# Optimization experiments

Hardware: AMD Instinct MI355X
Metric: run time of the kernel (lower is better)

The kernel has to match this reference:

```python
import math
import jax, jax.numpy as jnp
import numpy as np

H = 8
C_HIDDEN = 32
C_Q = 256


def setup_inputs() -> dict:
    key = jax.random.key(0)
    ks = jax.random.split(key, 9)
    B, S, Q, K = 1, 128, 256, 256
    q_x = jax.random.normal(ks[0], (B, S, Q, C_Q), dtype=jnp.float32)
    kv_x = jax.random.normal(ks[1], (B, S, K, C_Q), dtype=jnp.float32)
    bias1 = jax.random.normal(ks[2], (B, S, 1, 1, K), dtype=jnp.float32)
    bias2 = jax.random.normal(ks[3], (B, 1, H, Q, K), dtype=jnp.float32)
    scale = 1.0 / math.sqrt(C_Q)
    wq = jax.random.normal(ks[4], (H * C_HIDDEN, C_Q), dtype=jnp.float32) * scale
    wk = jax.random.normal(ks[5], (H * C_HIDDEN, C_Q), dtype=jnp.float32) * scale
    wv = jax.random.normal(ks[6], (H * C_HIDDEN, C_Q), dtype=jnp.float32) * scale
    wg = jax.random.normal(ks[7], (H * C_HIDDEN, C_Q), dtype=jnp.float32) * scale
    wo = jax.random.normal(ks[8], (C_Q, H * C_HIDDEN), dtype=jnp.float32) * scale
    return {"q_x": q_x, "kv_x": kv_x, "bias1": bias1, "bias2": bias2,
            "wq": wq, "wk": wk, "wv": wv, "wg": wg, "wo": wo}


def _split_heads(x):
    # [..., L, H*c] -> [..., H, L, c]
    y = x.reshape(x.shape[:-1] + (H, C_HIDDEN))
    return jnp.moveaxis(y, -2, -3)


def reference(q_x, kv_x, bias1, bias2, wq, wk, wv, wg, wo):
    # QKV projections (no bias), per-head split, scale q by 1/sqrt(c_hidden)
    q = _split_heads(q_x @ wq.T) / math.sqrt(C_HIDDEN)   # [B,S,H,Q,c]
    k = _split_heads(kv_x @ wk.T)                         # [B,S,H,K,c]
    v = _split_heads(kv_x @ wv.T)                         # [B,S,H,K,c]
    # attention logits with additive biases folded in
    a = jnp.einsum('...hqc,...hkc->...hqk', q, k) + bias1 + bias2
    a = jax.nn.softmax(a, axis=-1)
    o = jnp.einsum('...hqk,...hkc->...hqc', a, v)         # [B,S,H,Q,c]
    o = jnp.moveaxis(o, -3, -2)                           # [B,S,Q,H,c]
    # sigmoid gating from query data
    g = jax.nn.sigmoid(q_x @ wg.T)                        # [B,S,Q,H*c]
    g = g.reshape(g.shape[:-1] + (H, C_HIDDEN))
    o = o * g
    o = o.reshape(o.shape[:-2] + (H * C_HIDDEN,))         # flatten heads
    return o @ wo.T                                       # [B,S,Q,C_Q]
```

## Files before the change

### kernel.cpp

```cpp
#include <hip/hip_runtime.h>
#include <math.h>

#define S_DIM 128
#define H_DIM 8
#define M_TOT (S_DIM * 256)

typedef unsigned short ushort_t;
typedef unsigned int   uint32;
typedef __bf16  v8bf  __attribute__((ext_vector_type(8)));
typedef float   v4f   __attribute__((ext_vector_type(4)));

__device__ inline ushort_t f2b(float x) {
    unsigned int u = __float_as_uint(x);
    u += 0x7fffu + ((u >> 16) & 1u);
    return (ushort_t)(u >> 16);
}
__device__ inline float b2f(ushort_t h) {
    return __uint_as_float(((unsigned int)h) << 16);
}

#define GLDS16(gp, lp) __builtin_amdgcn_global_load_lds( \
    (const __attribute__((address_space(1))) void*)(gp), \
    (__attribute__((address_space(3))) void*)(lp), 16, 0, 0)

__global__ __launch_bounds__(256) void split_x(
    const float* __restrict__ xq, const float* __restrict__ xkv,
    ushort_t* __restrict__ hi, ushort_t* __restrict__ lo)
{
    const size_t BUF4 = (size_t)M_TOT * 64;
    const float* src = blockIdx.y ? xkv : xq;
    size_t base = (size_t)blockIdx.y * BUF4;
    int i = blockIdx.x * 256 + threadIdx.x;
    float4 v = ((const float4*)src)[i];
    ushort4 h, l;
    h.x = f2b(v.x); l.x = f2b(v.x - b2f(h.x));
    h.y = f2b(v.y); l.y = f2b(v.y - b2f(h.y));
    h.z = f2b(v.z); l.z = f2b(v.z - b2f(h.z));
    h.w = f2b(v.w); l.w = f2b(v.w - b2f(h.w));
    ((ushort4*)hi)[base + i] = h;
    ((ushort4*)lo)[base + i] = l;
}

__global__ __launch_bounds__(256) void split_w(
    const float* __restrict__ w0, const float* __restrict__ w1,
    const float* __restrict__ w2, const float* __restrict__ w3,
    const float* __restrict__ w4,
    ushort_t* __restrict__ hi, ushort_t* __restrict__ lo)
{
    const float* src;
    switch (blockIdx.y) {
        case 0: src = w0; break; case 1: src = w1; break;
        case 2: src = w2; break; case 3: src = w3; break;
        default: src = w4; break;
    }
    int i = blockIdx.x * 256 + threadIdx.x;
    float4 v = ((const float4*)src)[i];
    ushort4 h, l;
    h.x = f2b(v.x); l.x = f2b(v.x - b2f(h.x));
    h.y = f2b(v.y); l.y = f2b(v.y - b2f(h.y));
    h.z = f2b(v.z); l.z = f2b(v.z - b2f(h.z));
    h.w = f2b(v.w); l.w = f2b(v.w - b2f(h.w));
    size_t base = (size_t)blockIdx.y * 16384;
    ((ushort4*)hi)[base + i] = h;
    ((ushort4*)lo)[base + i] = l;
}


__global__ __launch_bounds__(256) void gemm_proj(
    const ushort_t* __restrict__ Xhi, const ushort_t* __restrict__ Xlo,
    const ushort_t* __restrict__ Whi4, const ushort_t* __restrict__ Wlo4,
    ushort_t* __restrict__ qh, ushort_t* __restrict__ ql,
    ushort_t* __restrict__ kh, ushort_t* __restrict__ kl,
    float* __restrict__ g_out,
    ushort_t* __restrict__ vh,
    float qscale)
{
    __shared__ ushort_t lds[4][128 * 32];

    const int z    = blockIdx.z;
    const int L    = blockIdx.x + 4 * blockIdx.y;
    const int mti  = ((L >> 5) << 3) + (L & 7);
    const int nti  = (L >> 3) & 3;
    const int t    = threadIdx.x;
    const int l    = t & 63;
    const int wv   = t >> 6;
    const int wm   = wv & 1;
    const int wn   = wv >> 1;
    const int idx  = l & 15;
    const int quad = l >> 4;
    const int m0   = mti * 128;
    const int n0   = nti * 128;

    const size_t BUF = (size_t)M_TOT * 256;
    const ushort_t* Ahi = Xhi + (size_t)z * BUF;
    const ushort_t* Alo = Xlo + (size_t)z * BUF;
    const ushort_t* Whi = Whi4 + (size_t)z * 131072;
    const ushort_t* Wlo = Wlo4 + (size_t)z * 131072;
    const float scale = z ? 1.f : qscale;

    const ushort_t* srcs[4] = { Ahi + (size_t)m0 * 256, Alo + (size_t)m0 * 256,
                                Whi + (size_t)n0 * 256, Wlo + (size_t)n0 * 256 };

    v4f acc[4][4];
    #pragma unroll
    for (int i = 0; i < 4; ++i)
        #pragma unroll
        for (int j = 0; j < 4; ++j) acc[i][j] = (v4f){0.f, 0.f, 0.f, 0.f};

    for (int k0 = 0; k0 < 256; k0 += 32) {
        #pragma unroll
        for (int b = 0; b < 4; ++b) {
            #pragma unroll
            for (int i = 0; i < 2; ++i) {
                const int sb   = wv * 128 + i * 64;
                const int slot = sb + l;
                const int row  = slot >> 2;
                const int gseg = ((slot & 3) - (row >> 1)) & 3;
                const ushort_t* g = srcs[b] + (size_t)row * 256 + k0 + gseg * 8;
                GLDS16(g, &lds[b][sb * 8]);
            }
        }
        __builtin_amdgcn_s_waitcnt(0);
        __syncthreads();

        v8bf ah[4], al[4], bh[4], bl[4];
        #pragma unroll
        for (int mt = 0; mt < 4; ++mt) {
            const int r   = wm * 64 + mt * 16 + idx;
            const int off = r * 32 + (((quad + (r >> 1)) & 3) << 3);
            ah[mt] = *(const v8bf*)&lds[0][off];
            al[mt] = *(const v8bf*)&lds[1][off];
        }
        #pragma unroll
        for (int nt = 0; nt < 4; ++nt) {
            const int r   = wn * 64 + nt * 16 + idx;
            const int off = r * 32 + (((quad + (r >> 1)) & 3) << 3);
            bh[nt] = *(const v8bf*)&lds[2][off];
            bl[nt] = *(const v8bf*)&lds[3][off];
        }

        #pragma unroll
        for (int mt = 0; mt < 4; ++mt)
            #pragma unroll
            for (int nt = 0; nt < 4; ++nt) {
                acc[mt][nt] = __builtin_amdgcn_mfma_f32_16x16x32_bf16(ah[mt], bh[nt], acc[mt][nt], 0, 0, 0);
                acc[mt][nt] = __builtin_amdgcn_mfma_f32_16x16x32_bf16(al[mt], bh[nt], acc[mt][nt], 0, 0, 0);
                acc[mt][nt] = __builtin_amdgcn_mfma_f32_16x16x32_bf16(ah[mt], bl[nt], acc[mt][nt], 0, 0, 0);
            }
        __syncthreads();
    }

    ushort_t* dsth = z ? kh : qh;
    ushort_t* dstl = z ? kl : ql;

    #pragma unroll
    for (int mt = 0; mt < 4; ++mt) {
        const int mbase = m0 + wm * 64 + mt * 16 + quad * 4;
        const int s = mbase >> 8, r8 = mbase & 255;
        #pragma unroll
        for (int nt = 0; nt < 4; ++nt) {
            const int gcol = n0 + wn * 64 + nt * 16 + idx;
            if (gcol < 256) {
                const int hh = gcol >> 5, c = gcol & 31;
                const size_t di = (((size_t)(s * 8 + hh) * 256) + r8) * 32 + c;
                #pragma unroll
                for (int r = 0; r < 4; ++r) {
                    const float val = acc[mt][nt][r] * scale;
                    const ushort_t hv = f2b(val);
                    dsth[di + (size_t)r * 32] = hv;
                    dstl[di + (size_t)r * 32] = f2b(val - b2f(hv));
                }
            } else if (z == 0) {
                const int gc = gcol - 256;
                #pragma unroll
                for (int r = 0; r < 4; ++r)
                    g_out[(size_t)(mbase + r) * 256 + gc] = acc[mt][nt][r];
            } else {
                const int gc = gcol - 256, hh = gc >> 5, c = gc & 31;
                ushort4 hv4;
                #pragma unroll
                for (int r = 0; r < 4; ++r)
                    ((ushort_t*)&hv4)[r] = f2b(acc[mt][nt][r]);
                const size_t di = (((size_t)(s * 8 + hh) * 32) + c) * 256 + r8;
                *(ushort4*)&vh[di] = hv4;
            }
        }
    }
}

__global__ __launch_bounds__(256) void gemm_out(
    const ushort_t* __restrict__ Ah, const ushort_t* __restrict__ Whi,
    const ushort_t* __restrict__ Wlo, float* __restrict__ Cf)
{
    __shared__ ushort_t lds[3][128 * 32];

    const int L    = blockIdx.x + 2 * blockIdx.y;
    const int mti  = ((L >> 4) << 3) + (L & 7);
    const int nti  = (L >> 3) & 1;
    const int t    = threadIdx.x;
    const int l    = t & 63;
    const int wv   = t >> 6;
    const int wm   = wv & 1;
    const int wn   = wv >> 1;
    const int idx  = l & 15;
    const int quad = l >> 4;
    const int m0   = mti * 128;
    const int n0   = nti * 128;

    const ushort_t* srcs[3] = { Ah + (size_t)m0 * 256,
                                Whi + (size_t)n0 * 256, Wlo + (size_t)n0 * 256 };

    v4f acc[4][4];
    #pragma unroll
    for (int i = 0; i < 4; ++i)
        #pragma unroll
        for (int j = 0; j < 4; ++j) acc[i][j] = (v4f){0.f, 0.f, 0.f, 0.f};

    for (int k0 = 0; k0 < 256; k0 += 32) {
        #pragma unroll
        for (int b = 0; b < 3; ++b) {
            #pragma unroll
            for (int i = 0; i < 2; ++i) {
                const int sb   = wv * 128 + i * 64;
                const int slot = sb + l;
                const int row  = slot >> 2;
                const int gseg = ((slot & 3) - (row >> 1)) & 3;
                const ushort_t* g = srcs[b] + (size_t)row * 256 + k0 + gseg * 8;
                GLDS16(g, &lds[b][sb * 8]);
            }
        }
        __builtin_amdgcn_s_waitcnt(0);
        __syncthreads();

        v8bf ah[4], bh[4], bl[4];
        #pragma unroll
        for (int mt = 0; mt < 4; ++mt) {
            const int r   = wm * 64 + mt * 16 + idx;
            const int off = r * 32 + (((quad + (r >> 1)) & 3) << 3);
            ah[mt] = *(const v8bf*)&lds[0][off];
        }
        #pragma unroll
        for (int nt = 0; nt < 4; ++nt) {
            const int r   = wn * 64 + nt * 16 + idx;
            const int off = r * 32 + (((quad + (r >> 1)) & 3) << 3);
            bh[nt] = *(const v8bf*)&lds[1][off];
            bl[nt] = *(const v8bf*)&lds[2][off];
        }

        #pragma unroll
        for (int mt = 0; mt < 4; ++mt)
            #pragma unroll
            for (int nt = 0; nt < 4; ++nt) {
                acc[mt][nt] = __builtin_amdgcn_mfma_f32_16x16x32_bf16(ah[mt], bh[nt], acc[mt][nt], 0, 0, 0);
                acc[mt][nt] = __builtin_amdgcn_mfma_f32_16x16x32_bf16(ah[mt], bl[nt], acc[mt][nt], 0, 0, 0);
            }
        __syncthreads();
    }

    #pragma unroll
    for (int mt = 0; mt < 4; ++mt) {
        #pragma unroll
        for (int nt = 0; nt < 4; ++nt) {
            const int gcol = n0 + wn * 64 + nt * 16 + idx;
            #pragma unroll
            for (int r = 0; r < 4; ++r) {
                const int grow = m0 + wm * 64 + mt * 16 + quad * 4 + r;
                Cf[(size_t)grow * 256 + gcol] = acc[mt][nt][r];
            }
        }
    }
}

__global__ __launch_bounds__(256, 2) void attn_mfma(
    const ushort_t* __restrict__ qh, const ushort_t* __restrict__ ql,
    const ushort_t* __restrict__ kh, const ushort_t* __restrict__ kl,
    const ushort_t* __restrict__ vth,
    const float* __restrict__ b1, const float* __restrict__ b2,
    const float* __restrict__ gbuf,
    ushort_t* __restrict__ oh)
{
    __shared__ __align__(16) uint32 pbuf[4][64 * 36];
    __shared__ __align__(16) float  lbuf[4][64 * 4];
    __shared__ __align__(16) float  invl[4][64];

    const int sh = blockIdx.x, s = sh >> 3, h = sh & 7;
    const int t = threadIdx.x, l = t & 63, w = t >> 6;
    const int idx = l & 15, quad = l >> 4;

    const size_t shb = (size_t)sh * 8192;
    const ushort_t* qhp = qh + shb;
    const ushort_t* qlp = ql + shb;
    const ushort_t* khp = kh + shb;
    const ushort_t* klp = kl + shb;
    const ushort_t* vhp = vth + shb;
    const float* b1p = b1 + (size_t)s * 256;
    const float* b2p = b2 + (size_t)h * 65536;

    v8bf qfh[4], qfl[4];
    #pragma unroll
    for (int nt = 0; nt < 4; ++nt) {
        const int off = (w * 64 + nt * 16 + idx) * 32 + quad * 8;
        qfh[nt] = *(const v8bf*)(qhp + off);
        qfl[nt] = *(const v8bf*)(qlp + off);
    }

    v4f oacc[4][2];
    #pragma unroll
    for (int mt = 0; mt < 4; ++mt) {
        oacc[mt][0] = (v4f){0.f, 0.f, 0.f, 0.f};
        oacc[mt][1] = (v4f){0.f, 0.f, 0.f, 0.f};
    }
    float lrun[4] = {0.f, 0.f, 0.f, 0.f};

    for (int c4 = 0; c4 < 4; ++c4) {
        const int ak0 = c4 * 64;

        v8bf kfh[4], kfl[4];
        #pragma unroll
        for (int at = 0; at < 4; ++at) {
            const int off = (ak0 + at * 16 + idx) * 32 + quad * 8;
            kfh[at] = *(const v8bf*)(khp + off);
            kfl[at] = *(const v8bf*)(klp + off);
        }

        v4f sacc[4][4];
        #pragma unroll
        for (int at = 0; at < 4; ++at)
            #pragma unroll
            for (int nt = 0; nt < 4; ++nt)
                sacc[at][nt] = (v4f){0.f, 0.f, 0.f, 0.f};
        #pragma unroll
        for (int at = 0; at < 4; ++at)
            #pragma unroll
            for (int nt = 0; nt < 4; ++nt) {
                sacc[at][nt] = __builtin_amdgcn_mfma_f32_16x16x32_bf16(kfh[at], qfh[nt], sacc[at][nt], 0, 0, 0);
                sacc[at][nt] = __builtin_amdgcn_mfma_f32_16x16x32_bf16(kfl[at], qfh[nt], sacc[at][nt], 0, 0, 0);
                sacc[at][nt] = __builtin_amdgcn_mfma_f32_16x16x32_bf16(kfh[at], qfl[nt], sacc[at][nt], 0, 0, 0);
            }

        v4f b1v[4];
        #pragma unroll
        for (int at = 0; at < 4; ++at)
            b1v[at] = *(const v4f*)(b1p + ak0 + at * 16 + quad * 4);

        #pragma unroll
        for (int at = 0; at < 4; ++at)
            #pragma unroll
            for (int nt = 0; nt < 4; ++nt) {
                const int q = w * 64 + nt * 16 + idx;
                v4f b2v = *(const v4f*)(b2p + (size_t)q * 256 + ak0 + at * 16 + quad * 4);
                float e0 = __expf(b1v[at][0] + b2v[0] + sacc[at][nt][0]);
                float e1 = __expf(b1v[at][1] + b2v[1] + sacc[at][nt][1]);
                float e2 = __expf(b1v[at][2] + b2v[2] + sacc[at][nt][2]);
                float e3 = __expf(b1v[at][3] + b2v[3] + sacc[at][nt][3]);
                lrun[nt] += (e0 + e1) + (e2 + e3);
                uint32 p0 = __builtin_amdgcn_perm(__float_as_uint(e1) + 0x8000u,
                                                  __float_as_uint(e0) + 0x8000u, 0x07060302u);
                uint32 p1 = __builtin_amdgcn_perm(__float_as_uint(e3) + 0x8000u,
                                                  __float_as_uint(e2) + 0x8000u, 0x07060302u);
                const int dw = (nt * 16 + idx) * 36 + at * 8 + quad * 2;
                *(uint2*)&pbuf[w][dw] = make_uint2(p0, p1);
            }

        v8bf vfh[2][2];
        #pragma unroll
        for (int n2 = 0; n2 < 2; ++n2)
            #pragma unroll
            for (int kt = 0; kt < 2; ++kt) {
                const int off = (n2 * 16 + idx) * 256 + ak0 + kt * 32 + quad * 8;
                vfh[n2][kt] = *(const v8bf*)(vhp + off);
            }

        #pragma unroll
        for (int mt = 0; mt < 4; ++mt)
            #pragma unroll
            for (int kt = 0; kt < 2; ++kt) {
                v8bf pf = *(const v8bf*)&pbuf[w][(mt * 16 + idx) * 36 + kt * 16 + quad * 4];
                #pragma unroll
                for (int n2 = 0; n2 < 2; ++n2)
                    oacc[mt][n2] = __builtin_amdgcn_mfma_f32_16x16x32_bf16(pf, vfh[n2][kt], oacc[mt][n2], 0, 0, 0);
            }
    }

    #pragma unroll
    for (int nt = 0; nt < 4; ++nt)
        lbuf[w][(nt * 16 + idx) * 4 + quad] = lrun[nt];
    {
        v4f lv = *(const v4f*)&lbuf[w][l * 4];
        invl[w][l] = 1.f / ((lv[0] + lv[1]) + (lv[2] + lv[3]));
    }

    #pragma unroll
    for (int mt = 0; mt < 4; ++mt) {
        v4f iv = *(const v4f*)&invl[w][mt * 16 + quad * 4];
        #pragma unroll
        for (int n2 = 0; n2 < 2; ++n2) {
            const int c = n2 * 16 + idx;
            #pragma unroll
            for (int r = 0; r < 4; ++r) {
                const int q = w * 64 + mt * 16 + quad * 4 + r;
                const size_t gi = (size_t)(s * 256 + q) * 256 + h * 32 + c;
                const float gv = gbuf[gi];
                const float sig = 1.f / (1.f + __expf(-gv));
                oh[gi] = f2b(oacc[mt][n2][r] * iv[r] * sig);
            }
        }
    }
}

extern "C" void kernel_launch(void* const* d_in, const int* in_sizes, int n_in,
                              void* d_out, int out_size, void* d_ws, size_t ws_size,
                              hipStream_t stream)
{
    const float* q_x   = (const float*)d_in[0];
    const float* kv_x  = (const float*)d_in[1];
    const float* bias1 = (const float*)d_in[2];
    const float* bias2 = (const float*)d_in[3];
    const float* wq    = (const float*)d_in[4];
    const float* wk    = (const float*)d_in[5];
    const float* wv    = (const float*)d_in[6];
    const float* wg    = (const float*)d_in[7];
    const float* wo    = (const float*)d_in[8];
    float* out = (float*)d_out;

    const size_t BUF = (size_t)M_TOT * 256;

    float*    g_buf = (float*)d_ws;
    ushort_t* p     = (ushort_t*)(g_buf + BUF);
    ushort_t* qhb = p;            ushort_t* qlb = qhb + BUF;
    ushort_t* khb = qlb + BUF;    ushort_t* klb = khb + BUF;
    ushort_t* vhb = klb + BUF;
    ushort_t* ohb = vhb + BUF;
    ushort_t* xhb = ohb + BUF;    ushort_t* xlb = xhb + 2 * BUF;
    ushort_t* w_hi = xlb + 2 * BUF;
    ushort_t* w_lo = w_hi + 5 * 65536;

    const float qscale = 0.17677669529663689f;

    split_w<<<dim3(64, 5), 256, 0, stream>>>(wq, wg, wk, wv, wo, w_hi, w_lo);

    split_x<<<dim3(8192, 2), 256, 0, stream>>>(q_x, kv_x, xhb, xlb);

    gemm_proj<<<dim3(4, 256, 2), 256, 0, stream>>>(
        xhb, xlb, w_hi, w_lo, qhb, qlb, khb, klb, g_buf, vhb, qscale);

    attn_mfma<<<S_DIM * H_DIM, 256, 0, stream>>>(
        qhb, qlb, khb, klb, vhb, bias1, bias2, g_buf, ohb);

    gemm_out<<<dim3(2, 256), 256, 0, stream>>>(
        ohb, w_hi + 4 * 65536, w_lo + 4 * 65536, out);
}
```

Before: 285.6 us.

## Double-buffer K fragments, hoist V loads, raise MFMA priority, shuffle-reduce row sums

The attention kernel now prefetches the next chunk's K fragments into a double-buffered register set and issues the V fragment loads at the top of each chunk, so global-load latency can overlap the QK and PV MFMAs. The MFMA sections are wrapped in s_setprio to favor matrix issue, and the loop is fully unrolled. The softmax row-sum reduction uses cross-lane xor shuffles instead of an LDS staging buffer. Extra live registers for the prefetched fragments may push register pressure against the two-blocks-per-CU launch bound.

```diff
diff --git a/kernel.cpp b/kernel.cpp
--- a/kernel.cpp
+++ b/kernel.cpp
@@ -280,7 +280,6 @@
     ushort_t* __restrict__ oh)
 {
     __shared__ __align__(16) uint32 pbuf[4][64 * 36];
-    __shared__ __align__(16) float  lbuf[4][64 * 4];
     __shared__ __align__(16) float  invl[4][64];
 
     const int sh = blockIdx.x, s = sh >> 3, h = sh & 7;
@@ -312,16 +311,36 @@
     }
     float lrun[4] = {0.f, 0.f, 0.f, 0.f};
 
+    v8bf kbh[2][4], kbl[2][4];
+    #pragma unroll
+    for (int at = 0; at < 4; ++at) {
+        const int off = (at * 16 + idx) * 32 + quad * 8;
+        kbh[0][at] = *(const v8bf*)(khp + off);
+        kbl[0][at] = *(const v8bf*)(klp + off);
+    }
+
+    #pragma unroll
     for (int c4 = 0; c4 < 4; ++c4) {
         const int ak0 = c4 * 64;
-
-        v8bf kfh[4], kfl[4];
-        #pragma unroll
-        for (int at = 0; at < 4; ++at) {
-            const int off = (ak0 + at * 16 + idx) * 32 + quad * 8;
-            kfh[at] = *(const v8bf*)(khp + off);
-            kfl[at] = *(const v8bf*)(klp + off);
-        }
+        const int cur = c4 & 1;
+
+        if (c4 < 3) {
+            #pragma unroll
+            for (int at = 0; at < 4; ++at) {
+                const int off = (ak0 + 64 + at * 16 + idx) * 32 + quad * 8;
+                kbh[cur ^ 1][at] = *(const v8bf*)(khp + off);
+                kbl[cur ^ 1][at] = *(const v8bf*)(klp + off);
+            }
+        }
+
+        v8bf vfh[2][2];
+        #pragma unroll
+        for (int n2 = 0; n2 < 2; ++n2)
+            #pragma unroll
+            for (int kt = 0; kt < 2; ++kt) {
+                const int off = (n2 * 16 + idx) * 256 + ak0 + kt * 32 + quad * 8;
+                vfh[n2][kt] = *(const v8bf*)(vhp + off);
+            }
 
         v4f sacc[4][4];
         #pragma unroll
@@ -329,14 +348,16 @@
             #pragma unroll
             for (int nt = 0; nt < 4; ++nt)
                 sacc[at][nt] = (v4f){0.f, 0.f, 0.f, 0.f};
+        __builtin_amdgcn_s_setprio(1);
         #pragma unroll
         for (int at = 0; at < 4; ++at)
             #pragma unroll
             for (int nt = 0; nt < 4; ++nt) {
-                sacc[at][nt] = __builtin_amdgcn_mfma_f32_16x16x32_bf16(kfh[at], qfh[nt], sacc[at][nt], 0, 0, 0);
-                sacc[at][nt] = __builtin_amdgcn_mfma_f32_16x16x32_bf16(kfl[at], qfh[nt], sacc[at][nt], 0, 0, 0);
-                sacc[at][nt] = __builtin_amdgcn_mfma_f32_16x16x32_bf16(kfh[at], qfl[nt], sacc[at][nt], 0, 0, 0);
-            }
+                sacc[at][nt] = __builtin_amdgcn_mfma_f32_16x16x32_bf16(kbh[cur][at], qfh[nt], sacc[at][nt], 0, 0, 0);
+                sacc[at][nt] = __builtin_amdgcn_mfma_f32_16x16x32_bf16(kbl[cur][at], qfh[nt], sacc[at][nt], 0, 0, 0);
+                sacc[at][nt] = __builtin_amdgcn_mfma_f32_16x16x32_bf16(kbh[cur][at], qfl[nt], sacc[at][nt], 0, 0, 0);
+            }
+        __builtin_amdgcn_s_setprio(0);
 
         v4f b1v[4];
         #pragma unroll
@@ -362,15 +383,7 @@
                 *(uint2*)&pbuf[w][dw] = make_uint2(p0, p1);
             }
 
-        v8bf vfh[2][2];
-        #pragma unroll
-        for (int n2 = 0; n2 < 2; ++n2)
-            #pragma unroll
-            for (int kt = 0; kt < 2; ++kt) {
-                const int off = (n2 * 16 + idx) * 256 + ak0 + kt * 32 + quad * 8;
-                vfh[n2][kt] = *(const v8bf*)(vhp + off);
-            }
-
+        __builtin_amdgcn_s_setprio(1);
         #pragma unroll
         for (int mt = 0; mt < 4; ++mt)
             #pragma unroll
@@ -380,14 +393,15 @@
                 for (int n2 = 0; n2 < 2; ++n2)
                     oacc[mt][n2] = __builtin_amdgcn_mfma_f32_16x16x32_bf16(pf, vfh[n2][kt], oacc[mt][n2], 0, 0, 0);
             }
-    }
-
-    #pragma unroll
-    for (int nt = 0; nt < 4; ++nt)
-        lbuf[w][(nt * 16 + idx) * 4 + quad] = lrun[nt];
-    {
-        v4f lv = *(const v4f*)&lbuf[w][l * 4];
-        invl[w][l] = 1.f / ((lv[0] + lv[1]) + (lv[2] + lv[3]));
+        __builtin_amdgcn_s_setprio(0);
+    }
+
+    #pragma unroll
+    for (int nt = 0; nt < 4; ++nt) {
+        float v = lrun[nt];
+        v += __shfl_xor(v, 16, 64);
+        v += __shfl_xor(v, 32, 64);
+        if (quad == 0) invl[w][nt * 16 + idx] = 1.f / v;
     }
 
     #pragma unroll
```

Result: slower. 310.5 us (+8.7%).
